# Kernel optimization log

Measured on AMD Instinct MI355X. Metric: run time of the kernel, lower is better.

## Reference

```python
import jax, jax.numpy as jnp
import numpy as np

EPS = 1e-5

def layer_norm(h, g, b):
    mu = h.mean(axis=-1, keepdims=True)
    var = jnp.mean((h - mu) ** 2, axis=-1, keepdims=True)
    return (h - mu) * jax.lax.rsqrt(var + EPS) * g + b

def setup_inputs() -> dict:
    key = jax.random.key(0)
    B, J, D, Ae, A, H, EH, LAT = 32, 16384, 32, 16, 4096, 128, 256, 32
    ks = jax.random.split(key, 12)
    in_dim = 1 + D + Ae  # 49
    inp = {
        "x": jax.random.normal(ks[0], (B, J), dtype=jnp.float32),
        "mask": jax.random.randint(ks[1], (B, J), 0, 2, dtype=jnp.int32),
        "atse_index": jax.random.randint(ks[2], (J,), 0, A, dtype=jnp.int32),
        "feature_embedding": jax.random.normal(ks[3], (J, D), dtype=jnp.float32),
        "atse_embedding": jax.random.normal(ks[4], (A, Ae), dtype=jnp.float32),
        # h_layer: Linear(in_dim->H) + LN + ReLU + Linear(H->D) + LN + ReLU
        "hW1": jax.random.normal(ks[5], (in_dim, H), dtype=jnp.float32) / np.sqrt(in_dim),
        "hb1": jnp.zeros((H,), jnp.float32),
        "hg1": jnp.ones((H,), jnp.float32),
        "hB1": jnp.zeros((H,), jnp.float32),
        "hW2": jax.random.normal(ks[6], (H, D), dtype=jnp.float32) / np.sqrt(H),
        "hb2": jnp.zeros((D,), jnp.float32),
        "hg2": jnp.ones((D,), jnp.float32),
        "hB2": jnp.zeros((D,), jnp.float32),
        # encoder_mlp (FCLayers, 2 layers, LayerNorm + ReLU each): D->EH->2*LAT
        "eW1": jax.random.normal(ks[7], (D, EH), dtype=jnp.float32) / np.sqrt(D),
        "eb1": jnp.zeros((EH,), jnp.float32),
        "eg1": jnp.ones((EH,), jnp.float32),
        "eB1": jnp.zeros((EH,), jnp.float32),
        "eW2": jax.random.normal(ks[8], (EH, 2 * LAT), dtype=jnp.float32) / np.sqrt(EH),
        "eb2": jnp.zeros((2 * LAT,), jnp.float32),
        "eg2": jnp.ones((2 * LAT,), jnp.float32),
        "eB2": jnp.zeros((2 * LAT,), jnp.float32),
    }
    return inp

def reference(x, mask, atse_index, feature_embedding, atse_embedding,
              hW1, hb1, hg1, hB1, hW2, hb2, hg2, hB2,
              eW1, eb1, eg1, eB1, eW2, eb2, eg2, eB2):
    B, J = x.shape
    Ae_per_j = atse_embedding[atse_index]  # [J, Ae] gather
    # h_in per (b, j): [psi | F_j | E_atse(j)] -> [B, J, 1+D+Ae]
    h_in = jnp.concatenate([
        x[:, :, None],
        jnp.broadcast_to(feature_embedding[None], (B,) + feature_embedding.shape),
        jnp.broadcast_to(Ae_per_j[None], (B,) + Ae_per_j.shape),
    ], axis=-1)
    h = jax.nn.relu(layer_norm(h_in @ hW1 + hb1, hg1, hB1))   # [B, J, H]
    h = jax.nn.relu(layer_norm(h @ hW2 + hb2, hg2, hB2))      # [B, J, D]
    m = mask.astype(h.dtype)                                   # [B, J]
    pooled = jnp.einsum('bj,bjd->bd', m, h)                    # masked sum pool
    cnt = m.sum(axis=-1, keepdims=True)
    c = pooled / jnp.maximum(cnt, 1.0)                         # mean; zero rows stay zero
    e = jax.nn.relu(layer_norm(c @ eW1 + eb1, eg1, eB1))
    ml = jax.nn.relu(layer_norm(e @ eW2 + eb2, eg2, eB2))      # [B, 2*latent]
    mu, logvar = jnp.split(ml, 2, axis=-1)
    return mu, logvar
```

## Files before the change

### kernel.cpp

```cpp
#include <hip/hip_runtime.h>
#include <hip/hip_bf16.h>

#define JTOT  16384
#define BATCH 32
#define DD    32
#define AE    16
#define HH    128
#define EHD   256
#define LATD  32
#define JT    16
#define NBLK  1024
#define EPSV  1e-5f

typedef __attribute__((ext_vector_type(8))) short short8;
typedef __attribute__((ext_vector_type(4))) float f32x4;
typedef __attribute__((ext_vector_type(2))) float v2f;

static __device__ __forceinline__ v2f mk2(float a, float b) {
    v2f r; r.x = a; r.y = b; return r;
}
static __device__ __forceinline__ v2f FMA2(v2f a, v2f b, v2f c) {
#if __has_builtin(__builtin_elementwise_fma)
    return __builtin_elementwise_fma(a, b, c);
#else
    v2f r; r.x = fmaf(a.x, b.x, c.x); r.y = fmaf(a.y, b.y, c.y); return r;
#endif
}
static __device__ __forceinline__ v2f MAX2(v2f a, v2f b) {
#if __has_builtin(__builtin_elementwise_max)
    return __builtin_elementwise_max(a, b);
#else
    v2f r; r.x = fmaxf(a.x, b.x); r.y = fmaxf(a.y, b.y); return r;
#endif
}

#define OFF_BASE 0
#define OFF_XS   2112
#define OFF_MS   2656
#define OFF_W0   3200
#define OFF_G1   3328
#define OFF_B1   3456
#define OFF_S0   3584
#define OFF_S1   3600
#define OFF_C1   3616
#define OFF_MW   3632
#define LDS_FLOATS 4224

__device__ __forceinline__ unsigned pk2(float lo, float hi) {
    float2 f; f.x = lo; f.y = hi;
    __hip_bfloat162 h = __float22bfloat162_rn(f);
    unsigned u; __builtin_memcpy(&u, &h, 4);
    return u;
}

__device__ __forceinline__ unsigned pke(v2f b, v2f w, v2f g, v2f Bl,
                                        float x, float rs, float cc) {
    v2f u = FMA2(mk2(x, x), w, b);
    v2f t = FMA2(u, mk2(rs, rs), mk2(cc, cc));
    v2f h = FMA2(t, g, Bl);
    h = MAX2(h, mk2(0.f, 0.f));
    return pk2(h.x, h.y);
}

__global__ __launch_bounds__(256, 2) void k_rows(
    const float* __restrict__ x, const int* __restrict__ mask,
    const int* __restrict__ aidx, const float* __restrict__ F,
    const float* __restrict__ AeE, const float* __restrict__ hW1,
    const float* __restrict__ hb1, const float* __restrict__ hg1,
    const float* __restrict__ hB1, const float* __restrict__ hW2,
    const float* __restrict__ hb2, const float* __restrict__ hg2,
    const float* __restrict__ hB2, float* __restrict__ partial)
{
    __shared__ float smem[LDS_FLOATS];
    const int tid = threadIdx.x;
    const int j0  = blockIdx.x * JT;

    float* BASEp = smem + OFF_BASE;
    float* XSp   = smem + OFF_XS;
    float* MSp   = smem + OFF_MS;
    float* W0p   = smem + OFF_W0;
    float* G1p   = smem + OFF_G1;
    float* B1p   = smem + OFF_B1;
    float* S0p   = smem + OFF_S0;
    float* S1p   = smem + OFF_S1;
    float* C1p   = smem + OFF_C1;
    float* MWp   = smem + OFF_MW;

    for (int o = tid; o < 512; o += 256) {
        int b = o >> 4, jj = o & 15;
        XSp[b * 17 + jj] = x[b * JTOT + j0 + jj];
        MSp[b * 17 + jj] = (float)mask[b * JTOT + j0 + jj];
    }
    if (tid < HH) { W0p[tid] = hW1[tid]; G1p[tid] = hg1[tid]; B1p[tid] = hB1[tid]; }

    {
        const int kk = tid & 127;
        const int jh = tid >> 7;
        float w[48];
        #pragma unroll
        for (int i = 0; i < 48; ++i) w[i] = hW1[(1 + i) * HH + kk];
        const float hb1v = hb1[kk];
        #pragma unroll
        for (int pr = 0; pr < 4; ++pr) {
            const int jja = 4 * pr + jh, jjb = jja + 2;
            const float4* Fa = (const float4*)(F + (j0 + jja) * DD);
            const float4* Fb = (const float4*)(F + (j0 + jjb) * DD);
            const float4* Aa = (const float4*)(AeE + aidx[j0 + jja] * AE);
            const float4* Ab = (const float4*)(AeE + aidx[j0 + jjb] * AE);
            v2f acc = mk2(hb1v, hb1v);
            #pragma unroll
            for (int i4 = 0; i4 < 8; ++i4) {
                float4 fa = Fa[i4], fb = Fb[i4];
                acc = FMA2(mk2(fa.x, fb.x), mk2(w[i4*4+0], w[i4*4+0]), acc);
                acc = FMA2(mk2(fa.y, fb.y), mk2(w[i4*4+1], w[i4*4+1]), acc);
                acc = FMA2(mk2(fa.z, fb.z), mk2(w[i4*4+2], w[i4*4+2]), acc);
                acc = FMA2(mk2(fa.w, fb.w), mk2(w[i4*4+3], w[i4*4+3]), acc);
            }
            #pragma unroll
            for (int i4 = 0; i4 < 4; ++i4) {
                float4 fa = Aa[i4], fb = Ab[i4];
                acc = FMA2(mk2(fa.x, fb.x), mk2(w[32+i4*4+0], w[32+i4*4+0]), acc);
                acc = FMA2(mk2(fa.y, fb.y), mk2(w[32+i4*4+1], w[32+i4*4+1]), acc);
                acc = FMA2(mk2(fa.z, fb.z), mk2(w[32+i4*4+2], w[32+i4*4+2]), acc);
                acc = FMA2(mk2(fa.w, fb.w), mk2(w[32+i4*4+3], w[32+i4*4+3]), acc);
            }
            BASEp[jja * 132 + kk] = acc.x;
            BASEp[jjb * 132 + kk] = acc.y;
        }
    }
    __syncthreads();

    {
        const int jj = tid >> 4, p = tid & 15;
        const float* bp = BASEp + jj * 132 + p * 8;
        const float* wp = W0p + p * 8;
        float s0 = 0.f, s1 = 0.f, c1 = 0.f;
        #pragma unroll
        for (int i = 0; i < 8; ++i) {
            float v = bp[i], wv = wp[i];
            s0 += v; s1 = fmaf(v, v, s1); c1 = fmaf(v, wv, c1);
        }
        #pragma unroll
        for (int m = 1; m < 16; m <<= 1) {
            s0 += __shfl_xor(s0, m); s1 += __shfl_xor(s1, m); c1 += __shfl_xor(c1, m);
        }
        if (p == 0) {
            S0p[jj] = s0 * (1.f / HH);
            S1p[jj] = s1 * (1.f / HH);
            C1p[jj] = c1 * (1.f / HH);
        }
    }
    if (tid < 64) {
        float a = W0p[tid], b = W0p[64 + tid];
        float s = a + b, qq = fmaf(a, a, b * b);
        #pragma unroll
        for (int m = 1; m < 64; m <<= 1) { s += __shfl_xor(s, m); qq += __shfl_xor(qq, m); }
        if (tid == 0) { MWp[0] = s * (1.f / HH); MWp[1] = qq * (1.f / HH); }
    }
    __syncthreads();

    const int lane = tid & 63;
    const int n = lane & 15, q = lane >> 4;
    const int wslot = tid >> 6;

    short8 Af[4][2];
    #pragma unroll
    for (int s = 0; s < 4; ++s)
        #pragma unroll
        for (int dt = 0; dt < 2; ++dt) {
            union { short8 v; unsigned u[4]; } t;
            #pragma unroll
            for (int p2 = 0; p2 < 4; ++p2) {
                int k0 = 32 * s + 8 * q + 2 * p2;
                t.u[p2] = pk2(hW2[(k0    ) * DD + dt * 16 + n],
                              hW2[(k0 + 1) * DD + dt * 16 + n]);
            }
            Af[s][dt] = t.v;
        }

    float hb2v[8], g2v[8], B2v[8];
    #pragma unroll
    for (int dt = 0; dt < 2; ++dt)
        #pragma unroll
        for (int r = 0; r < 4; ++r) {
            int d = dt * 16 + 4 * q + r;
            hb2v[dt*4+r] = hb2[d]; g2v[dt*4+r] = hg2[d]; B2v[dt*4+r] = hB2[d];
        }
    const float mw0v = MWp[0], sw0v = MWp[1];

    f32x4 pool[2][2];
    #pragma unroll
    for (int dt = 0; dt < 2; ++dt)
        #pragma unroll
        for (int bt = 0; bt < 2; ++bt)
            pool[dt][bt] = (f32x4){0.f, 0.f, 0.f, 0.f};

    #pragma unroll 1
    for (int jl = 0; jl < 4; ++jl) {
        const int jj = wslot * 4 + jl;
        const float x0  = XSp[n * 17 + jj];
        const float x1  = XSp[(16 + n) * 17 + jj];
        const float mv0 = MSp[n * 17 + jj];
        const float mv1 = MSp[(16 + n) * 17 + jj];
        const float S0 = S0p[jj], S1 = S1p[jj], C1 = C1p[jj];

        float mu0 = fmaf(x0, mw0v, S0);
        float e0  = fmaf(x0 * x0, sw0v, fmaf(2.f * x0, C1, S1));
        float rs0 = rsqrtf(fmaxf(e0 - mu0 * mu0, 0.f) + EPSV);
        float cc0 = -mu0 * rs0;
        float mu1 = fmaf(x1, mw0v, S0);
        float e1  = fmaf(x1 * x1, sw0v, fmaf(2.f * x1, C1, S1));
        float rs1 = rsqrtf(fmaxf(e1 - mu1 * mu1, 0.f) + EPSV);
        float cc1 = -mu1 * rs1;

        f32x4 Cacc[2][2];
        Cacc[0][0] = (f32x4){0.f,0.f,0.f,0.f}; Cacc[0][1] = (f32x4){0.f,0.f,0.f,0.f};
        Cacc[1][0] = (f32x4){0.f,0.f,0.f,0.f}; Cacc[1][1] = (f32x4){0.f,0.f,0.f,0.f};

        #pragma unroll
        for (int s = 0; s < 4; ++s) {
            const int off = 32 * s + 8 * q;
            const float* bp = BASEp + jj * 132 + off;
            union { short8 v; unsigned u[4]; } B0, B1;
            {
                float4 ba = *(const float4*)bp;
                float4 wa = *(const float4*)(W0p + off);
                float4 ga = *(const float4*)(G1p + off);
                float4 ca = *(const float4*)(B1p + off);
                B0.u[0] = pke(mk2(ba.x,ba.y), mk2(wa.x,wa.y), mk2(ga.x,ga.y), mk2(ca.x,ca.y), x0, rs0, cc0);
                B0.u[1] = pke(mk2(ba.z,ba.w), mk2(wa.z,wa.w), mk2(ga.z,ga.w), mk2(ca.z,ca.w), x0, rs0, cc0);
                B1.u[0] = pke(mk2(ba.x,ba.y), mk2(wa.x,wa.y), mk2(ga.x,ga.y), mk2(ca.x,ca.y), x1, rs1, cc1);
                B1.u[1] = pke(mk2(ba.z,ba.w), mk2(wa.z,wa.w), mk2(ga.z,ga.w), mk2(ca.z,ca.w), x1, rs1, cc1);
            }
            {
                float4 bb = *(const float4*)(bp + 4);
                float4 wb = *(const float4*)(W0p + off + 4);
                float4 gb = *(const float4*)(G1p + off + 4);
                float4 cb = *(const float4*)(B1p + off + 4);
                B0.u[2] = pke(mk2(bb.x,bb.y), mk2(wb.x,wb.y), mk2(gb.x,gb.y), mk2(cb.x,cb.y), x0, rs0, cc0);
                B0.u[3] = pke(mk2(bb.z,bb.w), mk2(wb.z,wb.w), mk2(gb.z,gb.w), mk2(cb.z,cb.w), x0, rs0, cc0);
                B1.u[2] = pke(mk2(bb.x,bb.y), mk2(wb.x,wb.y), mk2(gb.x,gb.y), mk2(cb.x,cb.y), x1, rs1, cc1);
                B1.u[3] = pke(mk2(bb.z,bb.w), mk2(wb.z,wb.w), mk2(gb.z,gb.w), mk2(cb.z,cb.w), x1, rs1, cc1);
            }
            Cacc[0][0] = __builtin_amdgcn_mfma_f32_16x16x32_bf16(Af[s][0], B0.v, Cacc[0][0], 0, 0, 0);
            Cacc[0][1] = __builtin_amdgcn_mfma_f32_16x16x32_bf16(Af[s][0], B1.v, Cacc[0][1], 0, 0, 0);
            Cacc[1][0] = __builtin_amdgcn_mfma_f32_16x16x32_bf16(Af[s][1], B0.v, Cacc[1][0], 0, 0, 0);
            Cacc[1][1] = __builtin_amdgcn_mfma_f32_16x16x32_bf16(Af[s][1], B1.v, Cacc[1][1], 0, 0, 0);
        }

        #pragma unroll
        for (int bt = 0; bt < 2; ++bt) {
            float v[8];
            float s = 0.f, ss = 0.f;
            #pragma unroll
            for (int dt = 0; dt < 2; ++dt)
                #pragma unroll
                for (int r = 0; r < 4; ++r) {
                    float t = Cacc[dt][bt][r] + hb2v[dt*4+r];
                    v[dt*4+r] = t;
                    s += t; ss = fmaf(t, t, ss);
                }
            s  += __shfl_xor(s, 16);  s  += __shfl_xor(s, 32);
            ss += __shfl_xor(ss, 16); ss += __shfl_xor(ss, 32);
            float mu  = s * (1.f / DD);
            float var = ss * (1.f / DD) - mu * mu;
            float rs  = rsqrtf(fmaxf(var, 0.f) + EPSV);
            float cc  = -mu * rs;
            float mv  = bt ? mv1 : mv0;
            #pragma unroll
            for (int dt = 0; dt < 2; ++dt)
                #pragma unroll
                for (int r = 0; r < 4; ++r) {
                    float t = fmaf(v[dt*4+r], rs, cc);
                    float h = fmaxf(fmaf(t, g2v[dt*4+r], B2v[dt*4+r]), 0.f);
                    pool[dt][bt][r] = fmaf(h, mv, pool[dt][bt][r]);
                }
        }
    }

    __syncthreads();
    #pragma unroll
    for (int dt = 0; dt < 2; ++dt)
        #pragma unroll
        for (int bt = 0; bt < 2; ++bt)
            #pragma unroll
            for (int r = 0; r < 4; ++r) {
                int d = dt * 16 + 4 * q + r, b = bt * 16 + n;
                smem[wslot * 1056 + b * 33 + d] = pool[dt][bt][r];
            }
    __syncthreads();
    for (int o = tid; o < 1024; o += 256) {
        int b = o >> 5, d = o & 31;
        int a = b * 33 + d;
        float sv = smem[a] + smem[1056 + a] + smem[2112 + a] + smem[3168 + a];
        partial[blockIdx.x * 1024 + o] = sv;
    }
}

__global__ __launch_bounds__(1024) void k_final(
    const float* __restrict__ partial, const int* __restrict__ mask,
    const float* __restrict__ eW1,
    const float* __restrict__ eb1, const float* __restrict__ eg1,
    const float* __restrict__ eB1,
    const float* __restrict__ eW2,
    const float* __restrict__ eb2, const float* __restrict__ eg2,
    const float* __restrict__ eB2,
    float* __restrict__ out, int nblk)
{
    const int b   = blockIdx.x;
    const int tid = threadIdx.x;

    __shared__ float red[32 * 32];
    __shared__ float cw[16], ws1[4], ws2[4];
    __shared__ float cS[DD];
    __shared__ float eS[EHD];

    {
        const int c = tid >> 5, d = tid & 31;
        float s = 0.f;
        for (int i = c; i < nblk; i += 32)
            s += partial[i * 1024 + b * 32 + d];
        red[c * 32 + d] = s;
    }
    {
        const int4* m4 = (const int4*)(mask + b * JTOT);
        float cs = 0.f;
        for (int i = tid; i < JTOT / 4; i += 1024) {
            int4 v = m4[i];
            cs += (float)(v.x + v.y + v.z + v.w);
        }
        #pragma unroll
        for (int m = 1; m < 64; m <<= 1) cs += __shfl_xor(cs, m);
        if ((tid & 63) == 0) cw[tid >> 6] = cs;
    }
    __syncthreads();

    if (tid < DD) {
        float c = 0.f;
        #pragma unroll
        for (int i = 0; i < 32; ++i) c += red[i * 32 + tid];
        float cnt = 0.f;
        #pragma unroll
        for (int i = 0; i < 16; ++i) cnt += cw[i];
        cS[tid] = c / fmaxf(cnt, 1.f);
    }
    __syncthreads();

    if (tid < EHD) {
        float e = eb1[tid];
        #pragma unroll
        for (int i = 0; i < DD; ++i) e = fmaf(cS[i], eW1[i * EHD + tid], e);
        float sum = e, ssq = e * e;
        #pragma unroll
        for (int m = 1; m < 64; m <<= 1) { sum += __shfl_xor(sum, m); ssq += __shfl_xor(ssq, m); }
        if ((tid & 63) == 0) { ws1[tid >> 6] = sum; ws2[tid >> 6] = ssq; }
        eS[tid] = e;
    }
    __syncthreads();
    if (tid < EHD) {
        float S1 = ws1[0] + ws1[1] + ws1[2] + ws1[3];
        float S2 = ws2[0] + ws2[1] + ws2[2] + ws2[3];
        float mu = S1 * (1.f / EHD);
        float var = S2 * (1.f / EHD) - mu * mu;
        float rs = rsqrtf(var + EPSV);
        eS[tid] = fmaxf(fmaf((eS[tid] - mu) * rs, eg1[tid], eB1[tid]), 0.f);
    }
    __syncthreads();

    if (tid < 2 * LATD) {
        float ml = eb2[tid];
        #pragma unroll 8
        for (int i = 0; i < EHD; ++i) ml = fmaf(eS[i], eW2[i * (2 * LATD) + tid], ml);
        float s = ml, qv = ml * ml;
        #pragma unroll
        for (int m = 1; m < 64; m <<= 1) { s += __shfl_xor(s, m); qv += __shfl_xor(qv, m); }
        float mu2 = s * (1.f / (2 * LATD));
        float var2 = qv * (1.f / (2 * LATD)) - mu2 * mu2;
        float rs2 = rsqrtf(var2 + EPSV);
        float v = fmaxf(fmaf((ml - mu2) * rs2, eg2[tid], eB2[tid]), 0.f);
        if (tid < LATD) out[b * LATD + tid] = v;
        else            out[BATCH * LATD + b * LATD + (tid - LATD)] = v;
    }
}

extern "C" void kernel_launch(void* const* d_in, const int* in_sizes, int n_in,
                              void* d_out, int out_size, void* d_ws, size_t ws_size,
                              hipStream_t stream) {
    const float* x    = (const float*)d_in[0];
    const int*   mask = (const int*)  d_in[1];
    const int*   aidx = (const int*)  d_in[2];
    const float* F    = (const float*)d_in[3];
    const float* AeE  = (const float*)d_in[4];
    const float* hW1  = (const float*)d_in[5];
    const float* hb1  = (const float*)d_in[6];
    const float* hg1  = (const float*)d_in[7];
    const float* hB1  = (const float*)d_in[8];
    const float* hW2  = (const float*)d_in[9];
    const float* hb2  = (const float*)d_in[10];
    const float* hg2  = (const float*)d_in[11];
    const float* hB2  = (const float*)d_in[12];
    const float* eW1  = (const float*)d_in[13];
    const float* eb1  = (const float*)d_in[14];
    const float* eg1  = (const float*)d_in[15];
    const float* eB1  = (const float*)d_in[16];
    const float* eW2  = (const float*)d_in[17];
    const float* eb2  = (const float*)d_in[18];
    const float* eg2  = (const float*)d_in[19];
    const float* eB2  = (const float*)d_in[20];
    float* out = (float*)d_out;

    float* partial = (float*)d_ws;

    k_rows<<<dim3(NBLK), dim3(256), 0, stream>>>(
        x, mask, aidx, F, AeE, hW1, hb1, hg1, hB1, hW2, hb2, hg2, hB2, partial);
    k_final<<<dim3(BATCH), dim3(1024), 0, stream>>>(
        partial, mask, eW1, eb1, eg1, eB1, eW2, eb2, eg2, eB2, out, NBLK);
}
```

Before: 152.4 us.

## Replace per-block partials with replicated atomic accumulators and single-block finalizer

Instead of writing 1024 per-block partial tiles that the final kernel re-reads, each row block atomically adds its pooled sums into one of 32 replicated accumulators, zeroed by a new small kernel. Mask counts are taken from values already staged in LDS in the main kernel, so the final kernel no longer re-reads the mask. The final encoder MLP runs in one 256-thread block handling 8 batches per wave. The aim is to cut the final kernel's memory traffic, at the cost of atomic contention, an extra launch, and a final stage with little parallelism.

```diff
diff --git a/kernel.cpp b/kernel.cpp
--- a/kernel.cpp
+++ b/kernel.cpp
@@ -11,6 +11,10 @@
 #define JT    16
 #define NBLK  1024
 #define EPSV  1e-5f
+
+#define WS_ACC   0
+#define WS_CNT   32768
+#define WS_TOTAL 33792
 
 typedef __attribute__((ext_vector_type(8))) short short8;
 typedef __attribute__((ext_vector_type(4))) float f32x4;
@@ -62,6 +66,11 @@
     return pk2(h.x, h.y);
 }
 
+__global__ __launch_bounds__(256) void k_zero(float* __restrict__ ws) {
+    int i = (blockIdx.x * 256 + threadIdx.x) * 4;
+    *(float4*)(ws + i) = (float4){0.f, 0.f, 0.f, 0.f};
+}
+
 __global__ __launch_bounds__(256, 2) void k_rows(
     const float* __restrict__ x, const int* __restrict__ mask,
     const int* __restrict__ aidx, const float* __restrict__ F,
@@ -69,7 +78,7 @@
     const float* __restrict__ hb1, const float* __restrict__ hg1,
     const float* __restrict__ hB1, const float* __restrict__ hW2,
     const float* __restrict__ hb2, const float* __restrict__ hg2,
-    const float* __restrict__ hB2, float* __restrict__ partial)
+    const float* __restrict__ hB2, float* __restrict__ ws)
 {
     __shared__ float smem[LDS_FLOATS];
     const int tid = threadIdx.x;
@@ -129,6 +138,12 @@
         }
     }
     __syncthreads();
+
+    float myCnt = 0.f;
+    if (tid < 32) {
+        #pragma unroll
+        for (int jj = 0; jj < JT; ++jj) myCnt += MSp[tid * 17 + jj];
+    }
 
     {
         const int jj = tid >> 4, p = tid & 15;
@@ -289,97 +304,117 @@
                 smem[wslot * 1056 + b * 33 + d] = pool[dt][bt][r];
             }
     __syncthreads();
+    const int rep = blockIdx.x & 31;
+    float* acc2 = ws + WS_ACC + rep * 1024;
     for (int o = tid; o < 1024; o += 256) {
         int b = o >> 5, d = o & 31;
         int a = b * 33 + d;
         float sv = smem[a] + smem[1056 + a] + smem[2112 + a] + smem[3168 + a];
-        partial[blockIdx.x * 1024 + o] = sv;
-    }
-}
-
-__global__ __launch_bounds__(1024) void k_final(
-    const float* __restrict__ partial, const int* __restrict__ mask,
+        atomicAdd(&acc2[o], sv);
+    }
+    if (tid < 32) atomicAdd(&ws[WS_CNT + rep * 32 + tid], myCnt);
+}
+
+__global__ __launch_bounds__(256) void k_final(
+    const float* __restrict__ ws,
     const float* __restrict__ eW1,
     const float* __restrict__ eb1, const float* __restrict__ eg1,
     const float* __restrict__ eB1,
     const float* __restrict__ eW2,
     const float* __restrict__ eb2, const float* __restrict__ eg2,
     const float* __restrict__ eB2,
-    float* __restrict__ out, int nblk)
+    float* __restrict__ out)
 {
-    const int b   = blockIdx.x;
-    const int tid = threadIdx.x;
-
-    __shared__ float red[32 * 32];
-    __shared__ float cw[16], ws1[4], ws2[4];
-    __shared__ float cS[DD];
-    __shared__ float eS[EHD];
-
+    const int tid  = threadIdx.x;
+    const int lane = tid & 63;
+    const int w    = tid >> 6;
+
+    __shared__ float cS[32 * 33];
+    __shared__ float cnS[32];
+    __shared__ float eSh[32 * 256];
+
+    if (tid < 32) {
+        float c = 0.f;
+        #pragma unroll
+        for (int r = 0; r < 32; ++r) c += ws[WS_CNT + r * 32 + tid];
+        cnS[tid] = fmaxf(c, 1.f);
+    }
+    __syncthreads();
+    for (int o = tid; o < 1024; o += 256) {
+        float s = 0.f;
+        #pragma unroll
+        for (int r = 0; r < 32; ++r) s += ws[WS_ACC + r * 1024 + o];
+        int b = o >> 5, d = o & 31;
+        cS[b * 33 + d] = s / cnS[b];
+    }
+    __syncthreads();
+
+    float e[8][4];
+    #pragma unroll
+    for (int i = 0; i < 4; ++i) {
+        float bi = eb1[64 * i + lane];
+        #pragma unroll
+        for (int bb = 0; bb < 8; ++bb) e[bb][i] = bi;
+    }
+    for (int d = 0; d < DD; ++d) {
+        float w4[4];
+        #pragma unroll
+        for (int i = 0; i < 4; ++i) w4[i] = eW1[d * EHD + 64 * i + lane];
+        #pragma unroll
+        for (int bb = 0; bb < 8; ++bb) {
+            float cv = cS[(8 * w + bb) * 33 + d];
+            #pragma unroll
+            for (int i = 0; i < 4; ++i) e[bb][i] = fmaf(cv, w4[i], e[bb][i]);
+        }
+    }
+    float g1v[4], B1v[4];
+    #pragma unroll
+    for (int i = 0; i < 4; ++i) { g1v[i] = eg1[64 * i + lane]; B1v[i] = eB1[64 * i + lane]; }
+
+    #pragma unroll
+    for (int bb = 0; bb < 8; ++bb) {
+        float s = 0.f, ss = 0.f;
+        #pragma unroll
+        for (int i = 0; i < 4; ++i) { s += e[bb][i]; ss = fmaf(e[bb][i], e[bb][i], ss); }
+        #pragma unroll
+        for (int m = 1; m < 64; m <<= 1) { s += __shfl_xor(s, m); ss += __shfl_xor(ss, m); }
+        float mu  = s * (1.f / EHD);
+        float var = ss * (1.f / EHD) - mu * mu;
+        float rs  = rsqrtf(var + EPSV);
+        float cc  = -mu * rs;
+        #pragma unroll
+        for (int i = 0; i < 4; ++i) {
+            float h = fmaxf(fmaf(fmaf(e[bb][i], rs, cc), g1v[i], B1v[i]), 0.f);
+            eSh[(w * 8 + bb) * 256 + 64 * i + lane] = h;
+        }
+    }
+    __syncthreads();
+
+    float ml[8];
     {
-        const int c = tid >> 5, d = tid & 31;
-        float s = 0.f;
-        for (int i = c; i < nblk; i += 32)
-            s += partial[i * 1024 + b * 32 + d];
-        red[c * 32 + d] = s;
-    }
-    {
-        const int4* m4 = (const int4*)(mask + b * JTOT);
-        float cs = 0.f;
-        for (int i = tid; i < JTOT / 4; i += 1024) {
-            int4 v = m4[i];
-            cs += (float)(v.x + v.y + v.z + v.w);
-        }
-        #pragma unroll
-        for (int m = 1; m < 64; m <<= 1) cs += __shfl_xor(cs, m);
-        if ((tid & 63) == 0) cw[tid >> 6] = cs;
-    }
-    __syncthreads();
-
-    if (tid < DD) {
-        float c = 0.f;
-        #pragma unroll
-        for (int i = 0; i < 32; ++i) c += red[i * 32 + tid];
-        float cnt = 0.f;
-        #pragma unroll
-        for (int i = 0; i < 16; ++i) cnt += cw[i];
-        cS[tid] = c / fmaxf(cnt, 1.f);
-    }
-    __syncthreads();
-
-    if (tid < EHD) {
-        float e = eb1[tid];
-        #pragma unroll
-        for (int i = 0; i < DD; ++i) e = fmaf(cS[i], eW1[i * EHD + tid], e);
-        float sum = e, ssq = e * e;
-        #pragma unroll
-        for (int m = 1; m < 64; m <<= 1) { sum += __shfl_xor(sum, m); ssq += __shfl_xor(ssq, m); }
-        if ((tid & 63) == 0) { ws1[tid >> 6] = sum; ws2[tid >> 6] = ssq; }
-        eS[tid] = e;
-    }
-    __syncthreads();
-    if (tid < EHD) {
-        float S1 = ws1[0] + ws1[1] + ws1[2] + ws1[3];
-        float S2 = ws2[0] + ws2[1] + ws2[2] + ws2[3];
-        float mu = S1 * (1.f / EHD);
-        float var = S2 * (1.f / EHD) - mu * mu;
-        float rs = rsqrtf(var + EPSV);
-        eS[tid] = fmaxf(fmaf((eS[tid] - mu) * rs, eg1[tid], eB1[tid]), 0.f);
-    }
-    __syncthreads();
-
-    if (tid < 2 * LATD) {
-        float ml = eb2[tid];
-        #pragma unroll 8
-        for (int i = 0; i < EHD; ++i) ml = fmaf(eS[i], eW2[i * (2 * LATD) + tid], ml);
-        float s = ml, qv = ml * ml;
-        #pragma unroll
-        for (int m = 1; m < 64; m <<= 1) { s += __shfl_xor(s, m); qv += __shfl_xor(qv, m); }
-        float mu2 = s * (1.f / (2 * LATD));
-        float var2 = qv * (1.f / (2 * LATD)) - mu2 * mu2;
-        float rs2 = rsqrtf(var2 + EPSV);
-        float v = fmaxf(fmaf((ml - mu2) * rs2, eg2[tid], eB2[tid]), 0.f);
-        if (tid < LATD) out[b * LATD + tid] = v;
-        else            out[BATCH * LATD + b * LATD + (tid - LATD)] = v;
+        float b2 = eb2[lane];
+        #pragma unroll
+        for (int bb = 0; bb < 8; ++bb) ml[bb] = b2;
+    }
+    for (int i = 0; i < EHD; ++i) {
+        float wv = eW2[i * (2 * LATD) + lane];
+        #pragma unroll
+        for (int bb = 0; bb < 8; ++bb)
+            ml[bb] = fmaf(eSh[(w * 8 + bb) * 256 + i], wv, ml[bb]);
+    }
+    float g2v = eg2[lane], B2v = eB2[lane];
+    #pragma unroll
+    for (int bb = 0; bb < 8; ++bb) {
+        int b = 8 * w + bb;
+        float s = ml[bb], ss = ml[bb] * ml[bb];
+        #pragma unroll
+        for (int m = 1; m < 64; m <<= 1) { s += __shfl_xor(s, m); ss += __shfl_xor(ss, m); }
+        float mu  = s * (1.f / (2 * LATD));
+        float var = ss * (1.f / (2 * LATD)) - mu * mu;
+        float rs  = rsqrtf(var + EPSV);
+        float v = fmaxf(fmaf(fmaf(ml[bb], rs, -mu * rs), g2v, B2v), 0.f);
+        if (lane < LATD) out[b * LATD + lane] = v;
+        else             out[BATCH * LATD + b * LATD + (lane - LATD)] = v;
     }
 }
 
@@ -408,11 +443,11 @@
     const float* eg2  = (const float*)d_in[19];
     const float* eB2  = (const float*)d_in[20];
     float* out = (float*)d_out;
-
-    float* partial = (float*)d_ws;
-
+    float* ws  = (float*)d_ws;
+
+    k_zero<<<dim3(WS_TOTAL / 1024), dim3(256), 0, stream>>>(ws);
     k_rows<<<dim3(NBLK), dim3(256), 0, stream>>>(
-        x, mask, aidx, F, AeE, hW1, hb1, hg1, hB1, hW2, hb2, hg2, hB2, partial);
-    k_final<<<dim3(BATCH), dim3(1024), 0, stream>>>(
-        partial, mask, eW1, eb1, eg1, eB1, eW2, eb2, eg2, eB2, out, NBLK);
-}
+        x, mask, aidx, F, AeE, hW1, hb1, hg1, hB1, hW2, hb2, hg2, hB2, ws);
+    k_final<<<dim3(1), dim3(256), 0, stream>>>(
+        ws, eW1, eb1, eg1, eB1, eW2, eb2, eg2, eB2, out);
+}
```

New measurement: 159.6 us. +4.8%, slower.
